# Performance work log

Measured on AMD Instinct MI355X. Metric: run time of the kernel, lower is better.

## Reference

```python
import jax, jax.numpy as jnp
import numpy as np


def setup_inputs() -> dict:
    key = jax.random.key(0)
    k1, k2 = jax.random.split(key)
    batch, dim = 16384, 1024
    x = jax.random.normal(k1, (batch, dim), dtype=jnp.float32)
    centers = jax.random.uniform(k2, (dim, dim), dtype=jnp.float32)  # matches torch.rand init
    return {"x": x, "centers": centers}


def reference(x, centers):
    # Pairwise squared distance ||x_b - c_k||^2 via the expanded form
    # (avoids the O(batch*dim*dim) diff tensor the torch code materializes).
    x_sq = jnp.sum(x * x, axis=-1, keepdims=True)          # [B, 1]
    c_sq = jnp.sum(centers * centers, axis=-1)             # [K]
    cross = jnp.einsum('bd,kd->bk', x, centers)            # [B, K]
    dist_sq = x_sq - 2.0 * cross + c_sq                    # [B, K]
    # output = log(softmax(-0.5 * dist_sq)) -> numerically stable log-softmax
    return jax.nn.log_softmax(-0.5 * dist_sq, axis=-1)
```

## Files before the change

kernel.cpp:

```cpp
#include <hip/hip_runtime.h>
#include <math.h>

typedef __attribute__((ext_vector_type(8))) short short8;
typedef __attribute__((ext_vector_type(4))) float f32x4;

__device__ inline short f2bf(float f) {
    unsigned u = __float_as_uint(f);
    u += 0x7FFFu + ((u >> 16) & 1u);
    return (short)(u >> 16);
}

__global__ __launch_bounds__(128) void cast_centers_frag(const float* __restrict__ c,
                                                         short* __restrict__ cbF,
                                                         float* __restrict__ chalf, int K) {
    const int n = blockIdx.x;
    const int i = threadIdx.x;
    const int k0 = i * 8;
    const float* row = c + (size_t)n * K;
    float4 a = *(const float4*)(row + k0);
    float4 b = *(const float4*)(row + k0 + 4);
    float s = a.x * a.x + a.y * a.y + a.z * a.z + a.w * a.w +
              b.x * b.x + b.y * b.y + b.z * b.z + b.w * b.w;
    short8 o;
    o[0] = f2bf(a.x); o[1] = f2bf(a.y); o[2] = f2bf(a.z); o[3] = f2bf(a.w);
    o[4] = f2bf(b.x); o[5] = f2bf(b.y); o[6] = f2bf(b.z); o[7] = f2bf(b.w);
    const size_t slab = (size_t)(K / 16) * 1024;
    const size_t addr = (size_t)(k0 >> 5) * slab + (size_t)(n >> 4) * 1024 +
                        (size_t)((n & 15) + ((k0 >> 3) & 3) * 16) * 16;
    *(short8*)((char*)cbF + addr) = o;
#pragma unroll
    for (int off = 32; off; off >>= 1) s += __shfl_xor(s, off);
    __shared__ float red[2];
    if ((i & 63) == 0) red[i >> 6] = s;
    __syncthreads();
    if (i == 0) chalf[n] = 0.5f * (red[0] + red[1]);
}

#define SCR 131072

__global__ __launch_bounds__(512, 2) void fused_kernel(
    const float* __restrict__ x,
    const short* __restrict__ cbF,
    const float* __restrict__ chalf,
    float* __restrict__ out,
    int M, int N, int K) {
    __shared__ char lds[131072 + 4608];
    const int t = threadIdx.x;
    const int l = t & 63, w = t >> 6, lr = l & 15, hi = l >> 4;
    const int brow = blockIdx.x * 64;

    {
        const int ar = t >> 3;
        const int cb8 = (t & 7) * 4;
        const float* xrow = x + (size_t)(brow + ar) * K;
        const int mb = (ar >> 4) * 1024 + (ar & 15) * 16;
#pragma unroll
        for (int j = 0; j < 32; ++j) {
            const int k0 = cb8 + j * 32;
            float4 v = *(const float4*)(xrow + k0);
            short4 p;
            p.x = f2bf(v.x); p.y = f2bf(v.y); p.z = f2bf(v.z); p.w = f2bf(v.w);
            *(short4*)(lds + (k0 >> 5) * 4096 + mb + (((k0 >> 3) & 3) << 8) + (k0 & 7) * 2) = p;
        }
    }
    __syncthreads();

    const char* bbase = (const char*)cbF + w * 8192 + l * 16;
    const int KS = K / 32;

    f32x4 acc[4][8];
#pragma unroll
    for (int m = 0; m < 4; ++m)
#pragma unroll
        for (int n = 0; n < 8; ++n)
#pragma unroll
            for (int q = 0; q < 4; ++q) acc[m][n][q] = 0.f;

#define LDB(dst, ks) do { _Pragma("unroll")                                      \
    for (int j = 0; j < 8; ++j)                                                  \
        dst[j] = *(const short8*)(bbase + (size_t)(ks) * 65536 + j * 1024); } while (0)

#define STEP(bset, ks) do {                                                      \
    short8 afr[4];                                                               \
    _Pragma("unroll")                                                            \
    for (int m = 0; m < 4; ++m)                                                  \
        afr[m] = *(const short8*)(lds + (ks) * 4096 + m * 1024 + l * 16);        \
    __builtin_amdgcn_s_setprio(1);                                               \
    _Pragma("unroll")                                                            \
    for (int m = 0; m < 4; ++m)                                                  \
        _Pragma("unroll")                                                        \
        for (int n = 0; n < 8; ++n)                                              \
            acc[m][n] = __builtin_amdgcn_mfma_f32_16x16x32_bf16(afr[m], bset[n], \
                                                                acc[m][n], 0, 0, 0); \
    __builtin_amdgcn_s_setprio(0); } while (0)

    short8 bE[8], bO[8];
    LDB(bE, 0);
    for (int k2 = 0; k2 < 15; ++k2) {
        LDB(bO, 2 * k2 + 1);
        STEP(bE, 2 * k2);
        LDB(bE, 2 * k2 + 2);
        STEP(bO, 2 * k2 + 1);
    }
    LDB(bO, 31);
    STEP(bE, 30);
    STEP(bO, 31);
#undef LDB
#undef STEP

    float ch[8];
#pragma unroll
    for (int n = 0; n < 8; ++n) ch[n] = chalf[w * 128 + n * 16 + lr];

    float pm[4][4];
#pragma unroll
    for (int m = 0; m < 4; ++m)
#pragma unroll
        for (int q = 0; q < 4; ++q) {
            float v = acc[m][0][q] - ch[0];
#pragma unroll
            for (int n = 1; n < 8; ++n) v = fmaxf(v, acc[m][n][q] - ch[n]);
            pm[m][q] = v;
        }
#pragma unroll
    for (int d = 1; d <= 8; d <<= 1)
#pragma unroll
        for (int m = 0; m < 4; ++m)
#pragma unroll
            for (int q = 0; q < 4; ++q) pm[m][q] = fmaxf(pm[m][q], __shfl_xor(pm[m][q], d));
    if (lr == 0) {
#pragma unroll
        for (int m = 0; m < 4; ++m)
#pragma unroll
            for (int q = 0; q < 4; ++q)
                *(float*)(lds + SCR + (m * 16 + hi * 4 + q) * 32 + w * 4) = pm[m][q];
    }
    __syncthreads();
    if (t < 64) {
        float4 a = *(const float4*)(lds + SCR + t * 32);
        float4 b = *(const float4*)(lds + SCR + t * 32 + 16);
        float g = fmaxf(fmaxf(fmaxf(a.x, a.y), fmaxf(a.z, a.w)),
                        fmaxf(fmaxf(b.x, b.y), fmaxf(b.z, b.w)));
        *(float*)(lds + SCR + 4096 + t * 4) = g;
    }
    __syncthreads();

    float ps[4][4];
#pragma unroll
    for (int m = 0; m < 4; ++m)
#pragma unroll
        for (int q = 0; q < 4; ++q) {
            const float g = *(const float*)(lds + SCR + 4096 + (m * 16 + hi * 4 + q) * 4);
            float s = 0.f;
#pragma unroll
            for (int n = 0; n < 8; ++n) s += __expf(acc[m][n][q] - ch[n] - g);
            ps[m][q] = s;
        }
#pragma unroll
    for (int d = 1; d <= 8; d <<= 1)
#pragma unroll
        for (int m = 0; m < 4; ++m)
#pragma unroll
            for (int q = 0; q < 4; ++q) ps[m][q] += __shfl_xor(ps[m][q], d);
    if (lr == 0) {
#pragma unroll
        for (int m = 0; m < 4; ++m)
#pragma unroll
            for (int q = 0; q < 4; ++q)
                *(float*)(lds + SCR + 2048 + (m * 16 + hi * 4 + q) * 32 + w * 4) = ps[m][q];
    }
    __syncthreads();
    if (t < 64) {
        float4 a = *(const float4*)(lds + SCR + 2048 + t * 32);
        float4 b = *(const float4*)(lds + SCR + 2048 + t * 32 + 16);
        float s = (a.x + a.y + a.z + a.w) + (b.x + b.y + b.z + b.w);
        *(float*)(lds + SCR + 4352 + t * 4) =
            *(const float*)(lds + SCR + 4096 + t * 4) + __logf(s);
    }
    __syncthreads();

#pragma unroll
    for (int m = 0; m < 4; ++m)
#pragma unroll
        for (int q = 0; q < 4; ++q) {
            const int R = m * 16 + hi * 4 + q;
            const float lse = *(const float*)(lds + SCR + 4352 + R * 4);
            float* orow = out + (size_t)(brow + R) * N + w * 128 + lr;
#pragma unroll
            for (int n = 0; n < 8; ++n)
                orow[n * 16] = acc[m][n][q] - ch[n] - lse;
        }
}

extern "C" void kernel_launch(void* const* d_in, const int* in_sizes, int n_in,
                              void* d_out, int out_size, void* d_ws, size_t ws_size,
                              hipStream_t stream) {
    const float* x = (const float*)d_in[0];
    const float* c = (const float*)d_in[1];
    float* out = (float*)d_out;

    int dim = (int)(sqrt((double)in_sizes[1]) + 0.5);
    int batch = in_sizes[0] / dim;

    size_t cb_bytes = (size_t)dim * dim * 2;
    short* cbF = (short*)d_ws;
    float* chalf = (float*)((char*)d_ws + cb_bytes);

    cast_centers_frag<<<dim, 128, 0, stream>>>(c, cbF, chalf, dim);

    fused_kernel<<<batch / 64, 512, 0, stream>>>(x, cbF, chalf, out, batch, dim, dim);
}
```

Before: 57.38 us.

## Triple-buffer center fragments and prefetch them before the x staging

The center-fragment register buffers go from two to three, so global loads run two k-steps ahead of the MFMA work, and the k-loop is fully unrolled. The first two B fragment sets are loaded before x is staged into LDS, so those global loads overlap the x load and bf16 conversion. The x staging also uses 8-float loads with 16-byte LDS stores instead of 4-float loads. The extra buffer adds 32 VGPRs per thread, which under the 512-thread, 2-block launch bound risks register spills or lower occupancy.

```diff
diff --git a/kernel.cpp b/kernel.cpp
--- a/kernel.cpp
+++ b/kernel.cpp
@@ -49,36 +49,41 @@
     const int l = t & 63, w = t >> 6, lr = l & 15, hi = l >> 4;
     const int brow = blockIdx.x * 64;
 
-    {
-        const int ar = t >> 3;
-        const int cb8 = (t & 7) * 4;
-        const float* xrow = x + (size_t)(brow + ar) * K;
-        const int mb = (ar >> 4) * 1024 + (ar & 15) * 16;
-#pragma unroll
-        for (int j = 0; j < 32; ++j) {
-            const int k0 = cb8 + j * 32;
-            float4 v = *(const float4*)(xrow + k0);
-            short4 p;
-            p.x = f2bf(v.x); p.y = f2bf(v.y); p.z = f2bf(v.z); p.w = f2bf(v.w);
-            *(short4*)(lds + (k0 >> 5) * 4096 + mb + (((k0 >> 3) & 3) << 8) + (k0 & 7) * 2) = p;
-        }
-    }
-    __syncthreads();
-
     const char* bbase = (const char*)cbF + w * 8192 + l * 16;
-    const int KS = K / 32;
-
-    f32x4 acc[4][8];
-#pragma unroll
-    for (int m = 0; m < 4; ++m)
-#pragma unroll
-        for (int n = 0; n < 8; ++n)
-#pragma unroll
-            for (int q = 0; q < 4; ++q) acc[m][n][q] = 0.f;
 
 #define LDB(dst, ks) do { _Pragma("unroll")                                      \
     for (int j = 0; j < 8; ++j)                                                  \
         dst[j] = *(const short8*)(bbase + (size_t)(ks) * 65536 + j * 1024); } while (0)
+
+    short8 B0[8], B1[8], B2[8];
+    LDB(B0, 0);
+    LDB(B1, 1);
+
+    {
+        const int ar = t >> 3;
+        const int c8 = t & 7;
+        const float* xrow = x + (size_t)(brow + ar) * K;
+        const int mb = (ar >> 4) * 1024 + (ar & 15) * 16;
+#pragma unroll
+        for (int j = 0; j < 16; ++j) {
+            const int k0 = c8 * 8 + j * 64;
+            float4 a = *(const float4*)(xrow + k0);
+            float4 b = *(const float4*)(xrow + k0 + 4);
+            short8 p;
+            p[0] = f2bf(a.x); p[1] = f2bf(a.y); p[2] = f2bf(a.z); p[3] = f2bf(a.w);
+            p[4] = f2bf(b.x); p[5] = f2bf(b.y); p[6] = f2bf(b.z); p[7] = f2bf(b.w);
+            *(short8*)(lds + (k0 >> 5) * 4096 + mb + (((k0 >> 3) & 3) << 8)) = p;
+        }
+    }
+    __syncthreads();
+
+    f32x4 acc[4][8];
+#pragma unroll
+    for (int m = 0; m < 4; ++m)
+#pragma unroll
+        for (int n = 0; n < 8; ++n)
+#pragma unroll
+            for (int q = 0; q < 4; ++q) acc[m][n][q] = 0.f;
 
 #define STEP(bset, ks) do {                                                      \
     short8 afr[4];                                                               \
@@ -94,17 +99,17 @@
                                                                 acc[m][n], 0, 0, 0); \
     __builtin_amdgcn_s_setprio(0); } while (0)
 
-    short8 bE[8], bO[8];
-    LDB(bE, 0);
-    for (int k2 = 0; k2 < 15; ++k2) {
-        LDB(bO, 2 * k2 + 1);
-        STEP(bE, 2 * k2);
-        LDB(bE, 2 * k2 + 2);
-        STEP(bO, 2 * k2 + 1);
-    }
-    LDB(bO, 31);
-    STEP(bE, 30);
-    STEP(bO, 31);
+#pragma unroll
+    for (int k3 = 0; k3 < 30; k3 += 3) {
+        LDB(B2, k3 + 2);
+        STEP(B0, k3);
+        LDB(B0, k3 + 3);
+        STEP(B1, k3 + 1);
+        LDB(B1, k3 + 4);
+        STEP(B2, k3 + 2);
+    }
+    STEP(B0, 30);
+    STEP(B1, 31);
 #undef LDB
 #undef STEP
 
```

Measured after the change: 57.61 us. Within noise of the previous version (+0.4%).

## Stream x tiles through a 4-slot LDS ring instead of staging full row block

Applied to the files above, without the earlier changes.

Instead of converting the block's whole 64x1024 x tile to bf16 into 128KB of LDS up front, the kernel now streams x in 32-wide K slices through a 4-slot LDS ring (16KB), software-pipelining the global loads and bf16 conversion with the MFMA loop. This removes the serial prologue load phase and cuts LDS usage so more blocks can be resident per CU. The cost is a barrier per K step and more careful register pressure from prefetched x and B fragments.

```diff
diff --git a/kernel.cpp b/kernel.cpp
--- a/kernel.cpp
+++ b/kernel.cpp
@@ -36,7 +36,7 @@
     if (i == 0) chalf[n] = 0.5f * (red[0] + red[1]);
 }
 
-#define SCR 131072
+#define SCR 16384
 
 __global__ __launch_bounds__(512, 2) void fused_kernel(
     const float* __restrict__ x,
@@ -44,69 +44,94 @@
     const float* __restrict__ chalf,
     float* __restrict__ out,
     int M, int N, int K) {
-    __shared__ char lds[131072 + 4608];
+    __shared__ char lds[16384 + 4608];
     const int t = threadIdx.x;
     const int l = t & 63, w = t >> 6, lr = l & 15, hi = l >> 4;
     const int brow = blockIdx.x * 64;
 
-    {
-        const int ar = t >> 3;
-        const int cb8 = (t & 7) * 4;
-        const float* xrow = x + (size_t)(brow + ar) * K;
-        const int mb = (ar >> 4) * 1024 + (ar & 15) * 16;
-#pragma unroll
-        for (int j = 0; j < 32; ++j) {
-            const int k0 = cb8 + j * 32;
-            float4 v = *(const float4*)(xrow + k0);
-            short4 p;
-            p.x = f2bf(v.x); p.y = f2bf(v.y); p.z = f2bf(v.z); p.w = f2bf(v.w);
-            *(short4*)(lds + (k0 >> 5) * 4096 + mb + (((k0 >> 3) & 3) << 8) + (k0 & 7) * 2) = p;
-        }
-    }
-    __syncthreads();
-
     const char* bbase = (const char*)cbF + w * 8192 + l * 16;
-    const int KS = K / 32;
-
-    f32x4 acc[4][8];
-#pragma unroll
-    for (int m = 0; m < 4; ++m)
-#pragma unroll
-        for (int n = 0; n < 8; ++n)
-#pragma unroll
-            for (int q = 0; q < 4; ++q) acc[m][n][q] = 0.f;
+
+    const int ar = t >> 3, c8 = t & 7;
+    const float* xsrc = x + (size_t)(brow + ar) * K + c8 * 4;
+    const int awofs = (ar >> 4) * 1024 + (ar & 15) * 16 + (c8 >> 1) * 256 + (c8 & 1) * 8;
 
 #define LDB(dst, ks) do { _Pragma("unroll")                                      \
     for (int j = 0; j < 8; ++j)                                                  \
         dst[j] = *(const short8*)(bbase + (size_t)(ks) * 65536 + j * 1024); } while (0)
 
-#define STEP(bset, ks) do {                                                      \
-    short8 afr[4];                                                               \
-    _Pragma("unroll")                                                            \
-    for (int m = 0; m < 4; ++m)                                                  \
-        afr[m] = *(const short8*)(lds + (ks) * 4096 + m * 1024 + l * 16);        \
+#define AW(ks, fv) do {                                                          \
+    short4 p_;                                                                   \
+    p_.x = f2bf((fv).x); p_.y = f2bf((fv).y);                                    \
+    p_.z = f2bf((fv).z); p_.w = f2bf((fv).w);                                    \
+    *(short4*)(lds + ((ks) & 3) * 4096 + awofs) = p_; } while (0)
+
+    f32x4 acc[4][8];
+#pragma unroll
+    for (int m = 0; m < 4; ++m)
+#pragma unroll
+        for (int n = 0; n < 8; ++n)
+#pragma unroll
+            for (int q = 0; q < 4; ++q) acc[m][n][q] = 0.f;
+
+    short8 Ba[8], Bb[8];
+    float4 xf0, xf1;
+
+    xf0 = *(const float4*)(xsrc);
+    xf1 = *(const float4*)(xsrc + 32);
+    LDB(Ba, 0);
+    AW(0, xf0);
+    AW(1, xf1);
+    xf0 = *(const float4*)(xsrc + 64);
+    xf1 = *(const float4*)(xsrc + 96);
+    LDB(Bb, 1);
+    asm volatile("s_waitcnt lgkmcnt(0)" ::: "memory");
+    __builtin_amdgcn_s_barrier();
+
+#define MFMACL(Bcur) do {                                                        \
     __builtin_amdgcn_s_setprio(1);                                               \
     _Pragma("unroll")                                                            \
     for (int m = 0; m < 4; ++m)                                                  \
         _Pragma("unroll")                                                        \
         for (int n = 0; n < 8; ++n)                                              \
-            acc[m][n] = __builtin_amdgcn_mfma_f32_16x16x32_bf16(afr[m], bset[n], \
+            acc[m][n] = __builtin_amdgcn_mfma_f32_16x16x32_bf16(af[m], Bcur[n],  \
                                                                 acc[m][n], 0, 0, 0); \
     __builtin_amdgcn_s_setprio(0); } while (0)
 
-    short8 bE[8], bO[8];
-    LDB(bE, 0);
-    for (int k2 = 0; k2 < 15; ++k2) {
-        LDB(bO, 2 * k2 + 1);
-        STEP(bE, 2 * k2);
-        LDB(bE, 2 * k2 + 2);
-        STEP(bO, 2 * k2 + 1);
-    }
-    LDB(bO, 31);
-    STEP(bE, 30);
-    STEP(bO, 31);
+#define AREAD(ks) short8 af[4];                                                  \
+    _Pragma("unroll")                                                            \
+    for (int m = 0; m < 4; ++m)                                                  \
+        af[m] = *(const short8*)(lds + ((ks) & 3) * 4096 + m * 1024 + l * 16);
+
+#define SYNCP() do {                                                             \
+    asm volatile("s_waitcnt lgkmcnt(0)" ::: "memory");                           \
+    __builtin_amdgcn_s_barrier();                                                \
+    __builtin_amdgcn_sched_barrier(0); } while (0)
+
+    for (int ks = 0; ks < 28; ks += 2) {
+        {
+            AREAD(ks); SYNCP();
+            MFMACL(Ba);
+            AW(ks + 2, xf0);
+            LDB(Ba, ks + 2);
+            xf0 = *(const float4*)(xsrc + (size_t)(ks + 4) * 32);
+        }
+        {
+            AREAD(ks + 1); SYNCP();
+            MFMACL(Bb);
+            AW(ks + 3, xf1);
+            LDB(Bb, ks + 3);
+            xf1 = *(const float4*)(xsrc + (size_t)(ks + 5) * 32);
+        }
+    }
+    { AREAD(28); SYNCP(); MFMACL(Ba); AW(30, xf0); LDB(Ba, 30); }
+    { AREAD(29); SYNCP(); MFMACL(Bb); AW(31, xf1); LDB(Bb, 31); }
+    { AREAD(30); SYNCP(); MFMACL(Ba); }
+    { AREAD(31); SYNCP(); MFMACL(Bb); }
+#undef AREAD
+#undef MFMACL
+#undef SYNCP
 #undef LDB
-#undef STEP
+#undef AW
 
     float ch[8];
 #pragma unroll
```

Result: faster. 55.39 us (-3.5%).
